# Performance work log

Measured on AMD Instinct MI355X. Metric: run time of the kernel, lower is better.

The kernel has to match this reference:

```python
import jax, jax.numpy as jnp
import numpy as np

B, L, S, H, E, D = 2, 2048, 2048, 8, 64, 64

def setup_inputs() -> dict:
    key = jax.random.key(0)
    kq, kk, kv = jax.random.split(key, 3)
    queries = jax.random.normal(kq, (B, L, H, E), dtype=jnp.float32)
    keys = jax.random.normal(kk, (B, S, H, E), dtype=jnp.float32)
    values = jax.random.normal(kv, (B, S, H, D), dtype=jnp.float32)
    return {"queries": queries, "keys": keys, "values": values}

def reference(queries, keys, values):
    # queries: [B,L,H,E], keys: [B,S,H,E], values: [B,S,H,D]
    E_ = queries.shape[-1]
    scale = 1.0 / jnp.sqrt(jnp.asarray(E_, dtype=queries.dtype))
    # scores: [B,H,L,S]
    scores = jnp.einsum('blhe,bshe->bhls', queries, keys)
    # mask_flag=False, use_relative_pos=False, dropout=0.0 -> identity
    A = jax.nn.softmax(scale * scores, axis=-1)
    # output: [B,L,H,D]
    V = jnp.einsum('bhls,bshd->blhd', A, values)
    return V
```

## Files before the change

### kernel.cpp

```cpp
#include <hip/hip_runtime.h>
#include <hip/hip_bf16.h>


#define SCL2 0.18033688011112042f

#if __has_builtin(__builtin_amdgcn_exp2f)
#define EXP2(x) __builtin_amdgcn_exp2f(x)
#else
#define EXP2(x) exp2f(x)
#endif

typedef __attribute__((ext_vector_type(8))) short bf16x8;
typedef __attribute__((ext_vector_type(4))) float f32x4;
typedef __attribute__((ext_vector_type(16))) float f32x16;

static constexpr int Bc = 2, Lc = 2048, Sc = 2048, Hc = 8, Ec = 64, Dc = 64;
static constexpr int ELEMS = Bc * Lc * Hc * Ec;

static __device__ __forceinline__ unsigned short bfb(float x) {
  union { __hip_bfloat16 h; unsigned short u; } c;
  c.h = __float2bfloat16(x);
  return c.u;
}
static __device__ __forceinline__ unsigned pkbf(float a, float b) {
  union { __hip_bfloat162 h; unsigned u; } c;
  c.h = __float22bfloat162_rn(make_float2(a, b));
  return c.u;
}
static __device__ __forceinline__ bf16x8 pack4(unsigned w0, unsigned w1,
                                               unsigned w2, unsigned w3) {
  union { unsigned u[4]; bf16x8 v; } c;
  c.u[0] = w0; c.u[1] = w1; c.u[2] = w2; c.u[3] = w3;
  return c.v;
}
static __device__ __forceinline__ void plswap(unsigned a, unsigned b,
                                              unsigned& o0, unsigned& o1, int hi) {
#if __has_builtin(__builtin_amdgcn_permlane32_swap)
  auto r = __builtin_amdgcn_permlane32_swap(a, b, false, false);
  o0 = r[0];
  o1 = r[1];
#else
  unsigned ax = (unsigned)__shfl_xor((int)a, 32);
  unsigned bx = (unsigned)__shfl_xor((int)b, 32);
  o0 = hi ? bx : a;
  o1 = hi ? b : ax;
#endif
}
static __device__ __forceinline__ float cross_half_sum(float x, int hi) {
  unsigned ua, ub;
  plswap(__float_as_uint(x), __float_as_uint(x), ua, ub, hi);
  return __uint_as_float(ua) + __uint_as_float(ub);
}

__global__ __launch_bounds__(256) void prep_kv_kernel(const float* __restrict__ K,
                                                      const float* __restrict__ V,
                                                      __hip_bfloat16* __restrict__ Kc,
                                                      __hip_bfloat16* __restrict__ Vt) {
  __shared__ __hip_bfloat16 tile[4][64][68];
  if (blockIdx.x < 1024) {
    int t = blockIdx.x * 256 + threadIdx.x;
    int f = t * 8;
    int e = f & 63;
    int h = (f >> 6) & 7;
    int s = (f >> 9) & 2047;
    int b = f >> 20;
    float4 v0 = *reinterpret_cast<const float4*>(K + f);
    float4 v1 = *reinterpret_cast<const float4*>(K + f + 4);
    int es = e >> 4, hi = (e >> 3) & 1;
    int kb = s >> 5, qi = s & 31;
    int o = ((b << 3) + h) * (Sc * 64) + kb * 2048 + es * 512 + hi * 256 + qi * 8;
    union { ushort u[8]; uint4 q; } pk;
    pk.u[0] = bfb(v0.x); pk.u[1] = bfb(v0.y); pk.u[2] = bfb(v0.z); pk.u[3] = bfb(v0.w);
    pk.u[4] = bfb(v1.x); pk.u[5] = bfb(v1.y); pk.u[6] = bfb(v1.z); pk.u[7] = bfb(v1.w);
    *reinterpret_cast<uint4*>(Kc + o) = pk.q;
  } else {
    const int w = threadIdx.x >> 6;
    const int lane = threadIdx.x & 63;
    const int task = (blockIdx.x - 1024) * 4 + w;
    const int st = task & 31;
    const int bh = task >> 5;
    const int s0 = st * 64;
    const int b = bh >> 3, h = bh & 7;
#pragma unroll 4
    for (int j = 0; j < 64; ++j) {
      float v = V[((b * Sc + s0 + j) * Hc + h) * 64 + lane];
      tile[w][j][lane] = __float2bfloat16(v);
    }
    __syncthreads();
    const int qi = lane & 31, hi = lane >> 5;
    __hip_bfloat16* Vb = Vt + bh * (Sc * 64);
#pragma unroll
    for (int kb2 = 0; kb2 < 2; ++kb2)
#pragma unroll
      for (int d0 = 0; d0 < 2; ++d0)
#pragma unroll
        for (int ks = 0; ks < 2; ++ks) {
          union { ushort u[8]; uint4 q; } pk;
#pragma unroll
          for (int j = 0; j < 8; ++j) {
            union { __hip_bfloat16 h; ushort u; } c;
            c.h = tile[w][kb2 * 32 + ks * 16 + hi * 8 + j][d0 * 32 + qi];
            pk.u[j] = c.u;
          }
          int o = ((s0 >> 5) + kb2) * 2048 + d0 * 1024 + ks * 512 + lane * 8;
          *reinterpret_cast<uint4*>(Vb + o) = pk.q;
        }
  }
}

static __device__ __forceinline__ void sm_fixed(f32x16& sc, float& l, int hi,
                                                bf16x8& pb0, bf16x8& pb1) {
#pragma unroll
  for (int r = 0; r < 16; ++r) sc[r] = EXP2(sc[r]);
  float r0 = (sc[0] + sc[1]) + (sc[2] + sc[3]);
  float r1 = (sc[4] + sc[5]) + (sc[6] + sc[7]);
  float r2 = (sc[8] + sc[9]) + (sc[10] + sc[11]);
  float r3 = (sc[12] + sc[13]) + (sc[14] + sc[15]);
  l += (r0 + r1) + (r2 + r3);

  unsigned c0, c1, c2, c3, y0, y1, y2, y3;
  c0 = pkbf(sc[0], sc[1]);  c1 = pkbf(sc[4], sc[5]);
  c2 = pkbf(sc[2], sc[3]);  c3 = pkbf(sc[6], sc[7]);
  plswap(c0, c1, y0, y2, hi);
  plswap(c2, c3, y1, y3, hi);
  pb0 = pack4(y0, y1, y2, y3);
  c0 = pkbf(sc[8], sc[9]);   c1 = pkbf(sc[12], sc[13]);
  c2 = pkbf(sc[10], sc[11]); c3 = pkbf(sc[14], sc[15]);
  plswap(c0, c1, y0, y2, hi);
  plswap(c2, c3, y1, y3, hi);
  pb1 = pack4(y0, y1, y2, y3);
}

__global__ __launch_bounds__(256, 2) void attn_kernel(const float* __restrict__ Qf32,
                                                      const __hip_bfloat16* __restrict__ Kc,
                                                      const __hip_bfloat16* __restrict__ Vt,
                                                      float* __restrict__ Out) {
  __shared__ float obuf[4][2][16][64];
  __shared__ float mlb[2][4][32];

  const int lid = blockIdx.x;
  const int xcd = lid & 7;
  const int i = lid >> 3;
  const int bh = (xcd << 1) | (i >> 5);
  const int q0 = (i & 31) << 6;
  const int w = threadIdx.x >> 6;
  const int lane = threadIdx.x & 63;
  const int qi = lane & 31;
  const int hi = lane >> 5;
  const int b = bh >> 3, h = bh & 7;

  const __hip_bfloat16* Kh = Kc + bh * (Sc * 64);
  const __hip_bfloat16* Vh = Vt + bh * (Sc * 64);

  bf16x8 qf[2][4];
#pragma unroll
  for (int g = 0; g < 2; ++g) {
    const float* qrow = Qf32 + ((b * Lc + q0 + g * 32 + qi) * Hc + h) * 64 + hi * 8;
#pragma unroll
    for (int es = 0; es < 4; ++es) {
      float4 a = *reinterpret_cast<const float4*>(qrow + es * 16);
      float4 c = *reinterpret_cast<const float4*>(qrow + es * 16 + 4);
      qf[g][es] = pack4(pkbf(a.x * SCL2, a.y * SCL2), pkbf(a.z * SCL2, a.w * SCL2),
                        pkbf(c.x * SCL2, c.y * SCL2), pkbf(c.z * SCL2, c.w * SCL2));
    }
  }

  f32x16 zero;
#pragma unroll
  for (int r = 0; r < 16; ++r) zero[r] = 0.f;

  f32x16 oa0 = zero, ob0 = zero, oa1 = zero, ob1 = zero;
  float l0 = 0.f, l1 = 0.f;

  bf16x8 kA0, kA1, kA2, kA3, kB0, kB1, kB2, kB3;

  auto loadK = [&](bf16x8& r0, bf16x8& r1, bf16x8& r2, bf16x8& r3, int t) {
    const __hip_bfloat16* Kp = Kh + (w + 4 * t) * 2048 + lane * 8;
    r0 = *reinterpret_cast<const bf16x8*>(Kp + 0 * 512);
    r1 = *reinterpret_cast<const bf16x8*>(Kp + 1 * 512);
    r2 = *reinterpret_cast<const bf16x8*>(Kp + 2 * 512);
    r3 = *reinterpret_cast<const bf16x8*>(Kp + 3 * 512);
  };

  auto body = [&](const bf16x8& k0, const bf16x8& k1, const bf16x8& k2, const bf16x8& k3,
                  bf16x8& n0, bf16x8& n1, bf16x8& n2, bf16x8& n3, int t, int tn) {
    const __hip_bfloat16* Vp = Vh + (w + 4 * t) * 2048 + lane * 8;
    bf16x8 v0 = *reinterpret_cast<const bf16x8*>(Vp + 0 * 512);
    bf16x8 v1 = *reinterpret_cast<const bf16x8*>(Vp + 1 * 512);
    bf16x8 v2 = *reinterpret_cast<const bf16x8*>(Vp + 2 * 512);
    bf16x8 v3 = *reinterpret_cast<const bf16x8*>(Vp + 3 * 512);

    f32x16 sc0, sc1;
    sc0 = __builtin_amdgcn_mfma_f32_32x32x16_bf16(k0, qf[0][0], zero, 0, 0, 0);
    sc0 = __builtin_amdgcn_mfma_f32_32x32x16_bf16(k1, qf[0][1], sc0, 0, 0, 0);
    sc0 = __builtin_amdgcn_mfma_f32_32x32x16_bf16(k2, qf[0][2], sc0, 0, 0, 0);
    sc0 = __builtin_amdgcn_mfma_f32_32x32x16_bf16(k3, qf[0][3], sc0, 0, 0, 0);
    sc1 = __builtin_amdgcn_mfma_f32_32x32x16_bf16(k0, qf[1][0], zero, 0, 0, 0);
    sc1 = __builtin_amdgcn_mfma_f32_32x32x16_bf16(k1, qf[1][1], sc1, 0, 0, 0);
    sc1 = __builtin_amdgcn_mfma_f32_32x32x16_bf16(k2, qf[1][2], sc1, 0, 0, 0);
    sc1 = __builtin_amdgcn_mfma_f32_32x32x16_bf16(k3, qf[1][3], sc1, 0, 0, 0);

    if (tn < 16) loadK(n0, n1, n2, n3, tn);

    bf16x8 pa0, pa1, pb0, pb1;
    sm_fixed(sc0, l0, hi, pa0, pa1);
    sm_fixed(sc1, l1, hi, pb0, pb1);

    oa0 = __builtin_amdgcn_mfma_f32_32x32x16_bf16(v0, pa0, oa0, 0, 0, 0);
    oa1 = __builtin_amdgcn_mfma_f32_32x32x16_bf16(v0, pb0, oa1, 0, 0, 0);
    oa0 = __builtin_amdgcn_mfma_f32_32x32x16_bf16(v1, pa1, oa0, 0, 0, 0);
    oa1 = __builtin_amdgcn_mfma_f32_32x32x16_bf16(v1, pb1, oa1, 0, 0, 0);
    ob0 = __builtin_amdgcn_mfma_f32_32x32x16_bf16(v2, pa0, ob0, 0, 0, 0);
    ob1 = __builtin_amdgcn_mfma_f32_32x32x16_bf16(v2, pb0, ob1, 0, 0, 0);
    ob0 = __builtin_amdgcn_mfma_f32_32x32x16_bf16(v3, pa1, ob0, 0, 0, 0);
    ob1 = __builtin_amdgcn_mfma_f32_32x32x16_bf16(v3, pb1, ob1, 0, 0, 0);
  };

  loadK(kA0, kA1, kA2, kA3, 0);
  for (int t = 0; t < 16; t += 2) {
    body(kA0, kA1, kA2, kA3, kB0, kB1, kB2, kB3, t, t + 1);
    body(kB0, kB1, kB2, kB3, kA0, kA1, kA2, kA3, t + 1, t + 2);
  }

  l0 = cross_half_sum(l0, hi);
  l1 = cross_half_sum(l1, hi);

  if (hi == 0) {
    mlb[0][w][qi] = l0;
    mlb[1][w][qi] = l1;
  }
  __syncthreads();
  float inv[2];
#pragma unroll
  for (int g = 0; g < 2; ++g)
    inv[g] = 1.0f / (mlb[g][0][qi] + mlb[g][1][qi] + mlb[g][2][qi] + mlb[g][3][qi]);

  const int d0 = w >> 1, rr = (w & 1) * 8;
#pragma unroll
  for (int g = 0; g < 2; ++g) {
    if (g) __syncthreads();
    const f32x16& A = g ? oa1 : oa0;
    const f32x16& Bv = g ? ob1 : ob0;
#pragma unroll
    for (int r = 0; r < 16; ++r) {
      obuf[w][0][r][lane] = A[r];
      obuf[w][1][r][lane] = Bv[r];
    }
    __syncthreads();
    float* orow = Out + ((b * Lc + q0 + g * 32 + qi) * Hc + h) * Dc;
#pragma unroll
    for (int t = 0; t < 2; ++t) {
      f32x4 acc;
#pragma unroll
      for (int j = 0; j < 4; ++j) {
        const int r = rr + 4 * t + j;
        acc[j] = (obuf[0][d0][r][lane] + obuf[1][d0][r][lane] +
                  obuf[2][d0][r][lane] + obuf[3][d0][r][lane]) * inv[g];
      }
      const int dbase = d0 * 32 + ((rr + 4 * t) >> 2) * 8 + hi * 4;
      *reinterpret_cast<f32x4*>(orow + dbase) = acc;
    }
  }
}

extern "C" void kernel_launch(void* const* d_in, const int* in_sizes, int n_in,
                              void* d_out, int out_size, void* d_ws, size_t ws_size,
                              hipStream_t stream) {
  const float* Q = (const float*)d_in[0];
  const float* K = (const float*)d_in[1];
  const float* V = (const float*)d_in[2];
  float* out = (float*)d_out;

  __hip_bfloat16* Kc = (__hip_bfloat16*)d_ws;
  __hip_bfloat16* Vt = Kc + ELEMS;

  prep_kv_kernel<<<dim3(1152), 256, 0, stream>>>(K, V, Kc, Vt);
  attn_kernel<<<dim3(512), 256, 0, stream>>>(Q, Kc, Vt, out);
}
```

Measured before the change: 40.68 us.

## Switch attention to fp16 MFMA, fdot2 row sums, smaller prep blocks, drop K prefetch

Changes the K/V/Q/P operands from bf16 to fp16 and uses the fp16 32x32x16 MFMA. The softmax row sum now comes from fdot2 on the packed fp16 probabilities instead of a float add tree. The prep kernel runs with 64-thread blocks, one wave each, so a block no longer waits on a barrier shared by four waves. The K double-buffer prefetch is removed and K is loaded inline, which shortens register live ranges but may expose load latency. fp16 probabilities and sums lose some range and exactness compared with fp32 sums.

```diff
diff --git a/kernel.cpp b/kernel.cpp
--- a/kernel.cpp
+++ b/kernel.cpp
@@ -1,5 +1,6 @@
 #include <hip/hip_runtime.h>
 #include <hip/hip_bf16.h>
+#include <hip/hip_fp16.h>
 
 
 #define SCL2 0.18033688011112042f
@@ -10,26 +11,27 @@
 #define EXP2(x) exp2f(x)
 #endif
 
-typedef __attribute__((ext_vector_type(8))) short bf16x8;
+typedef __attribute__((ext_vector_type(8))) _Float16 f16x8;
+typedef __attribute__((ext_vector_type(2))) _Float16 h2;
 typedef __attribute__((ext_vector_type(4))) float f32x4;
 typedef __attribute__((ext_vector_type(16))) float f32x16;
 
 static constexpr int Bc = 2, Lc = 2048, Sc = 2048, Hc = 8, Ec = 64, Dc = 64;
 static constexpr int ELEMS = Bc * Lc * Hc * Ec;
 
-static __device__ __forceinline__ unsigned short bfb(float x) {
-  union { __hip_bfloat16 h; unsigned short u; } c;
-  c.h = __float2bfloat16(x);
+static __device__ __forceinline__ unsigned short hfb(float x) {
+  union { __half h; unsigned short u; } c;
+  c.h = __float2half_rn(x);
   return c.u;
 }
-static __device__ __forceinline__ unsigned pkbf(float a, float b) {
-  union { __hip_bfloat162 h; unsigned u; } c;
-  c.h = __float22bfloat162_rn(make_float2(a, b));
+static __device__ __forceinline__ unsigned pkhf(float a, float b) {
+  union { __half2 h; unsigned u; } c;
+  c.h = __float22half2_rn(make_float2(a, b));
   return c.u;
 }
-static __device__ __forceinline__ bf16x8 pack4(unsigned w0, unsigned w1,
-                                               unsigned w2, unsigned w3) {
-  union { unsigned u[4]; bf16x8 v; } c;
+static __device__ __forceinline__ f16x8 pack4(unsigned w0, unsigned w1,
+                                              unsigned w2, unsigned w3) {
+  union { unsigned u[4]; f16x8 v; } c;
   c.u[0] = w0; c.u[1] = w1; c.u[2] = w2; c.u[3] = w3;
   return c.v;
 }
@@ -51,14 +53,25 @@
   plswap(__float_as_uint(x), __float_as_uint(x), ua, ub, hi);
   return __uint_as_float(ua) + __uint_as_float(ub);
 }
-
-__global__ __launch_bounds__(256) void prep_kv_kernel(const float* __restrict__ K,
-                                                      const float* __restrict__ V,
-                                                      __hip_bfloat16* __restrict__ Kc,
-                                                      __hip_bfloat16* __restrict__ Vt) {
-  __shared__ __hip_bfloat16 tile[4][64][68];
-  if (blockIdx.x < 1024) {
-    int t = blockIdx.x * 256 + threadIdx.x;
+static __device__ __forceinline__ float dot2acc(unsigned p, float l) {
+#if __has_builtin(__builtin_amdgcn_fdot2)
+  union { unsigned u; h2 v; } c; c.u = p;
+  h2 one = {(_Float16)1.0f, (_Float16)1.0f};
+  return __builtin_amdgcn_fdot2(c.v, one, l, false);
+#else
+  union { unsigned u; __half2 v; } c; c.u = p;
+  float2 f = __half22float2(c.v);
+  return l + f.x + f.y;
+#endif
+}
+
+__global__ __launch_bounds__(64) void prep_kv_kernel(const float* __restrict__ K,
+                                                     const float* __restrict__ V,
+                                                     __half* __restrict__ Kc,
+                                                     __half* __restrict__ Vt) {
+  __shared__ __half tile[64][68];
+  if (blockIdx.x < 4096) {
+    int t = blockIdx.x * 64 + threadIdx.x;
     int f = t * 8;
     int e = f & 63;
     int h = (f >> 6) & 7;
@@ -70,13 +83,12 @@
     int kb = s >> 5, qi = s & 31;
     int o = ((b << 3) + h) * (Sc * 64) + kb * 2048 + es * 512 + hi * 256 + qi * 8;
     union { ushort u[8]; uint4 q; } pk;
-    pk.u[0] = bfb(v0.x); pk.u[1] = bfb(v0.y); pk.u[2] = bfb(v0.z); pk.u[3] = bfb(v0.w);
-    pk.u[4] = bfb(v1.x); pk.u[5] = bfb(v1.y); pk.u[6] = bfb(v1.z); pk.u[7] = bfb(v1.w);
+    pk.u[0] = hfb(v0.x); pk.u[1] = hfb(v0.y); pk.u[2] = hfb(v0.z); pk.u[3] = hfb(v0.w);
+    pk.u[4] = hfb(v1.x); pk.u[5] = hfb(v1.y); pk.u[6] = hfb(v1.z); pk.u[7] = hfb(v1.w);
     *reinterpret_cast<uint4*>(Kc + o) = pk.q;
   } else {
-    const int w = threadIdx.x >> 6;
-    const int lane = threadIdx.x & 63;
-    const int task = (blockIdx.x - 1024) * 4 + w;
+    const int task = blockIdx.x - 4096;
+    const int lane = threadIdx.x;
     const int st = task & 31;
     const int bh = task >> 5;
     const int s0 = st * 64;
@@ -84,11 +96,11 @@
 #pragma unroll 4
     for (int j = 0; j < 64; ++j) {
       float v = V[((b * Sc + s0 + j) * Hc + h) * 64 + lane];
-      tile[w][j][lane] = __float2bfloat16(v);
+      tile[j][lane] = __float2half_rn(v);
     }
     __syncthreads();
     const int qi = lane & 31, hi = lane >> 5;
-    __hip_bfloat16* Vb = Vt + bh * (Sc * 64);
+    __half* Vb = Vt + bh * (Sc * 64);
 #pragma unroll
     for (int kb2 = 0; kb2 < 2; ++kb2)
 #pragma unroll
@@ -98,8 +110,8 @@
           union { ushort u[8]; uint4 q; } pk;
 #pragma unroll
           for (int j = 0; j < 8; ++j) {
-            union { __hip_bfloat16 h; ushort u; } c;
-            c.h = tile[w][kb2 * 32 + ks * 16 + hi * 8 + j][d0 * 32 + qi];
+            union { __half h; ushort u; } c;
+            c.h = tile[kb2 * 32 + ks * 16 + hi * 8 + j][d0 * 32 + qi];
             pk.u[j] = c.u;
           }
           int o = ((s0 >> 5) + kb2) * 2048 + d0 * 1024 + ks * 512 + lane * 8;
@@ -109,31 +121,27 @@
 }
 
 static __device__ __forceinline__ void sm_fixed(f32x16& sc, float& l, int hi,
-                                                bf16x8& pb0, bf16x8& pb1) {
+                                                f16x8& pb0, f16x8& pb1) {
 #pragma unroll
   for (int r = 0; r < 16; ++r) sc[r] = EXP2(sc[r]);
-  float r0 = (sc[0] + sc[1]) + (sc[2] + sc[3]);
-  float r1 = (sc[4] + sc[5]) + (sc[6] + sc[7]);
-  float r2 = (sc[8] + sc[9]) + (sc[10] + sc[11]);
-  float r3 = (sc[12] + sc[13]) + (sc[14] + sc[15]);
-  l += (r0 + r1) + (r2 + r3);
-
-  unsigned c0, c1, c2, c3, y0, y1, y2, y3;
-  c0 = pkbf(sc[0], sc[1]);  c1 = pkbf(sc[4], sc[5]);
-  c2 = pkbf(sc[2], sc[3]);  c3 = pkbf(sc[6], sc[7]);
+  unsigned c0, c1, c2, c3, d0, d1, d2, d3, y0, y1, y2, y3;
+  c0 = pkhf(sc[0], sc[1]);   c1 = pkhf(sc[4], sc[5]);
+  c2 = pkhf(sc[2], sc[3]);   c3 = pkhf(sc[6], sc[7]);
+  d0 = pkhf(sc[8], sc[9]);   d1 = pkhf(sc[12], sc[13]);
+  d2 = pkhf(sc[10], sc[11]); d3 = pkhf(sc[14], sc[15]);
+  l = dot2acc(c0, l); l = dot2acc(c1, l); l = dot2acc(c2, l); l = dot2acc(c3, l);
+  l = dot2acc(d0, l); l = dot2acc(d1, l); l = dot2acc(d2, l); l = dot2acc(d3, l);
   plswap(c0, c1, y0, y2, hi);
   plswap(c2, c3, y1, y3, hi);
   pb0 = pack4(y0, y1, y2, y3);
-  c0 = pkbf(sc[8], sc[9]);   c1 = pkbf(sc[12], sc[13]);
-  c2 = pkbf(sc[10], sc[11]); c3 = pkbf(sc[14], sc[15]);
-  plswap(c0, c1, y0, y2, hi);
-  plswap(c2, c3, y1, y3, hi);
+  plswap(d0, d1, y0, y2, hi);
+  plswap(d2, d3, y1, y3, hi);
   pb1 = pack4(y0, y1, y2, y3);
 }
 
 __global__ __launch_bounds__(256, 2) void attn_kernel(const float* __restrict__ Qf32,
-                                                      const __hip_bfloat16* __restrict__ Kc,
-                                                      const __hip_bfloat16* __restrict__ Vt,
+                                                      const __half* __restrict__ Kc,
+                                                      const __half* __restrict__ Vt,
                                                       float* __restrict__ Out) {
   __shared__ float obuf[4][2][16][64];
   __shared__ float mlb[2][4][32];
@@ -149,10 +157,10 @@
   const int hi = lane >> 5;
   const int b = bh >> 3, h = bh & 7;
 
-  const __hip_bfloat16* Kh = Kc + bh * (Sc * 64);
-  const __hip_bfloat16* Vh = Vt + bh * (Sc * 64);
-
-  bf16x8 qf[2][4];
+  const __half* Kh = Kc + bh * (Sc * 64);
+  const __half* Vh = Vt + bh * (Sc * 64);
+
+  f16x8 qf[2][4];
 #pragma unroll
   for (int g = 0; g < 2; ++g) {
     const float* qrow = Qf32 + ((b * Lc + q0 + g * 32 + qi) * Hc + h) * 64 + hi * 8;
@@ -160,8 +168,8 @@
     for (int es = 0; es < 4; ++es) {
       float4 a = *reinterpret_cast<const float4*>(qrow + es * 16);
       float4 c = *reinterpret_cast<const float4*>(qrow + es * 16 + 4);
-      qf[g][es] = pack4(pkbf(a.x * SCL2, a.y * SCL2), pkbf(a.z * SCL2, a.w * SCL2),
-                        pkbf(c.x * SCL2, c.y * SCL2), pkbf(c.z * SCL2, c.w * SCL2));
+      qf[g][es] = pack4(pkhf(a.x * SCL2, a.y * SCL2), pkhf(a.z * SCL2, a.w * SCL2),
+                        pkhf(c.x * SCL2, c.y * SCL2), pkhf(c.z * SCL2, c.w * SCL2));
     }
   }
 
@@ -172,54 +180,41 @@
   f32x16 oa0 = zero, ob0 = zero, oa1 = zero, ob1 = zero;
   float l0 = 0.f, l1 = 0.f;
 
-  bf16x8 kA0, kA1, kA2, kA3, kB0, kB1, kB2, kB3;
-
-  auto loadK = [&](bf16x8& r0, bf16x8& r1, bf16x8& r2, bf16x8& r3, int t) {
-    const __hip_bfloat16* Kp = Kh + (w + 4 * t) * 2048 + lane * 8;
-    r0 = *reinterpret_cast<const bf16x8*>(Kp + 0 * 512);
-    r1 = *reinterpret_cast<const bf16x8*>(Kp + 1 * 512);
-    r2 = *reinterpret_cast<const bf16x8*>(Kp + 2 * 512);
-    r3 = *reinterpret_cast<const bf16x8*>(Kp + 3 * 512);
-  };
-
-  auto body = [&](const bf16x8& k0, const bf16x8& k1, const bf16x8& k2, const bf16x8& k3,
-                  bf16x8& n0, bf16x8& n1, bf16x8& n2, bf16x8& n3, int t, int tn) {
-    const __hip_bfloat16* Vp = Vh + (w + 4 * t) * 2048 + lane * 8;
-    bf16x8 v0 = *reinterpret_cast<const bf16x8*>(Vp + 0 * 512);
-    bf16x8 v1 = *reinterpret_cast<const bf16x8*>(Vp + 1 * 512);
-    bf16x8 v2 = *reinterpret_cast<const bf16x8*>(Vp + 2 * 512);
-    bf16x8 v3 = *reinterpret_cast<const bf16x8*>(Vp + 3 * 512);
+  for (int t = 0; t < 16; ++t) {
+    const int tb = (w + 4 * t) * 2048 + lane * 8;
+    const __half* Kp = Kh + tb;
+    f16x8 k0 = *reinterpret_cast<const f16x8*>(Kp + 0 * 512);
+    f16x8 k1 = *reinterpret_cast<const f16x8*>(Kp + 1 * 512);
+    f16x8 k2 = *reinterpret_cast<const f16x8*>(Kp + 2 * 512);
+    f16x8 k3 = *reinterpret_cast<const f16x8*>(Kp + 3 * 512);
+    const __half* Vp = Vh + tb;
+    f16x8 v0 = *reinterpret_cast<const f16x8*>(Vp + 0 * 512);
+    f16x8 v1 = *reinterpret_cast<const f16x8*>(Vp + 1 * 512);
+    f16x8 v2 = *reinterpret_cast<const f16x8*>(Vp + 2 * 512);
+    f16x8 v3 = *reinterpret_cast<const f16x8*>(Vp + 3 * 512);
 
     f32x16 sc0, sc1;
-    sc0 = __builtin_amdgcn_mfma_f32_32x32x16_bf16(k0, qf[0][0], zero, 0, 0, 0);
-    sc0 = __builtin_amdgcn_mfma_f32_32x32x16_bf16(k1, qf[0][1], sc0, 0, 0, 0);
-    sc0 = __builtin_amdgcn_mfma_f32_32x32x16_bf16(k2, qf[0][2], sc0, 0, 0, 0);
-    sc0 = __builtin_amdgcn_mfma_f32_32x32x16_bf16(k3, qf[0][3], sc0, 0, 0, 0);
-    sc1 = __builtin_amdgcn_mfma_f32_32x32x16_bf16(k0, qf[1][0], zero, 0, 0, 0);
-    sc1 = __builtin_amdgcn_mfma_f32_32x32x16_bf16(k1, qf[1][1], sc1, 0, 0, 0);
-    sc1 = __builtin_amdgcn_mfma_f32_32x32x16_bf16(k2, qf[1][2], sc1, 0, 0, 0);
-    sc1 = __builtin_amdgcn_mfma_f32_32x32x16_bf16(k3, qf[1][3], sc1, 0, 0, 0);
-
-    if (tn < 16) loadK(n0, n1, n2, n3, tn);
-
-    bf16x8 pa0, pa1, pb0, pb1;
+    sc0 = __builtin_amdgcn_mfma_f32_32x32x16_f16(k0, qf[0][0], zero, 0, 0, 0);
+    sc0 = __builtin_amdgcn_mfma_f32_32x32x16_f16(k1, qf[0][1], sc0, 0, 0, 0);
+    sc0 = __builtin_amdgcn_mfma_f32_32x32x16_f16(k2, qf[0][2], sc0, 0, 0, 0);
+    sc0 = __builtin_amdgcn_mfma_f32_32x32x16_f16(k3, qf[0][3], sc0, 0, 0, 0);
+    sc1 = __builtin_amdgcn_mfma_f32_32x32x16_f16(k0, qf[1][0], zero, 0, 0, 0);
+    sc1 = __builtin_amdgcn_mfma_f32_32x32x16_f16(k1, qf[1][1], sc1, 0, 0, 0);
+    sc1 = __builtin_amdgcn_mfma_f32_32x32x16_f16(k2, qf[1][2], sc1, 0, 0, 0);
+    sc1 = __builtin_amdgcn_mfma_f32_32x32x16_f16(k3, qf[1][3], sc1, 0, 0, 0);
+
+    f16x8 pa0, pa1, pb0, pb1;
     sm_fixed(sc0, l0, hi, pa0, pa1);
     sm_fixed(sc1, l1, hi, pb0, pb1);
 
-    oa0 = __builtin_amdgcn_mfma_f32_32x32x16_bf16(v0, pa0, oa0, 0, 0, 0);
-    oa1 = __builtin_amdgcn_mfma_f32_32x32x16_bf16(v0, pb0, oa1, 0, 0, 0);
-    oa0 = __builtin_amdgcn_mfma_f32_32x32x16_bf16(v1, pa1, oa0, 0, 0, 0);
-    oa1 = __builtin_amdgcn_mfma_f32_32x32x16_bf16(v1, pb1, oa1, 0, 0, 0);
-    ob0 = __builtin_amdgcn_mfma_f32_32x32x16_bf16(v2, pa0, ob0, 0, 0, 0);
-    ob1 = __builtin_amdgcn_mfma_f32_32x32x16_bf16(v2, pb0, ob1, 0, 0, 0);
-    ob0 = __builtin_amdgcn_mfma_f32_32x32x16_bf16(v3, pa1, ob0, 0, 0, 0);
-    ob1 = __builtin_amdgcn_mfma_f32_32x32x16_bf16(v3, pb1, ob1, 0, 0, 0);
-  };
-
-  loadK(kA0, kA1, kA2, kA3, 0);
-  for (int t = 0; t < 16; t += 2) {
-    body(kA0, kA1, kA2, kA3, kB0, kB1, kB2, kB3, t, t + 1);
-    body(kB0, kB1, kB2, kB3, kA0, kA1, kA2, kA3, t + 1, t + 2);
+    oa0 = __builtin_amdgcn_mfma_f32_32x32x16_f16(v0, pa0, oa0, 0, 0, 0);
+    oa1 = __builtin_amdgcn_mfma_f32_32x32x16_f16(v0, pb0, oa1, 0, 0, 0);
+    oa0 = __builtin_amdgcn_mfma_f32_32x32x16_f16(v1, pa1, oa0, 0, 0, 0);
+    oa1 = __builtin_amdgcn_mfma_f32_32x32x16_f16(v1, pb1, oa1, 0, 0, 0);
+    ob0 = __builtin_amdgcn_mfma_f32_32x32x16_f16(v2, pa0, ob0, 0, 0, 0);
+    ob1 = __builtin_amdgcn_mfma_f32_32x32x16_f16(v2, pb0, ob1, 0, 0, 0);
+    ob0 = __builtin_amdgcn_mfma_f32_32x32x16_f16(v3, pa1, ob0, 0, 0, 0);
+    ob1 = __builtin_amdgcn_mfma_f32_32x32x16_f16(v3, pb1, ob1, 0, 0, 0);
   }
 
   l0 = cross_half_sum(l0, hi);
@@ -271,9 +266,9 @@
   const float* V = (const float*)d_in[2];
   float* out = (float*)d_out;
 
-  __hip_bfloat16* Kc = (__hip_bfloat16*)d_ws;
-  __hip_bfloat16* Vt = Kc + ELEMS;
-
-  prep_kv_kernel<<<dim3(1152), 256, 0, stream>>>(K, V, Kc, Vt);
+  __half* Kc = (__half*)d_ws;
+  __half* Vt = Kc + ELEMS;
+
+  prep_kv_kernel<<<dim3(4608), 64, 0, stream>>>(K, V, Kc, Vt);
   attn_kernel<<<dim3(512), 256, 0, stream>>>(Q, Kc, Vt, out);
 }
```

After: 40.00 us, median of 3. No clear change (-1.7%).
